# Kernel tuning notes

Measured on AMD Instinct MI355X. Metric: run time of the kernel, lower is better.

Reference implementation:

```python
import jax, jax.numpy as jnp
import numpy as np

N_NODES = 100000
EMBED_DIM = 128
N_EDGES = 3200000
K_HOPS = 2


def setup_inputs() -> dict:
    key = jax.random.key(0)
    k1, k2, k3, k4, k5, k6 = jax.random.split(key, 6)
    stdv = 1.0 / np.sqrt(EMBED_DIM)
    emb = jax.random.uniform(k1, (N_NODES, EMBED_DIM), jnp.float32, -stdv, stdv)
    emb = emb.at[0].set(0.0)  # padding_idx=0
    W = jax.random.uniform(k2, (EMBED_DIM, EMBED_DIM), jnp.float32, -stdv, stdv)
    b = jnp.zeros((EMBED_DIM,), jnp.float32)
    src = jax.random.randint(k3, (N_EDGES,), 0, N_NODES, jnp.int32)
    dst = jax.random.randint(k4, (N_EDGES,), 0, N_NODES, jnp.int32)
    neg_src = jax.random.randint(k5, (N_EDGES,), 0, N_NODES, jnp.int32)
    neg_dst = jax.random.randint(k6, (N_EDGES,), 0, N_NODES, jnp.int32)
    return {"emb": emb, "W": W, "b": b, "src": src, "dst": dst,
            "neg_src": neg_src, "neg_dst": neg_dst}


def _sgconv(x, src, dst, W, b):
    # DGL SGConv, norm='both': symmetric D^{-1/2} A D^{-1/2}, K hops, then Linear.
    deg = jax.ops.segment_sum(jnp.ones_like(dst, jnp.float32), dst,
                              num_segments=N_NODES)
    norm = jax.lax.rsqrt(jnp.maximum(deg, 1.0))[:, None]  # [N,1]
    h = x
    for _ in range(K_HOPS):
        h = h * norm
        h = jax.ops.segment_sum(h[src], dst, num_segments=N_NODES)
        h = h * norm
    return h @ W.T + b


def _edge_dot(h, s, d):
    # fn.u_dot_v: per-edge dot product -> [E,1]
    return jnp.sum(h[s] * h[d], axis=-1, keepdims=True)


def reference(emb, W, b, src, dst, neg_src, neg_dst):
    h = _sgconv(emb, src, dst, W, b)
    return _edge_dot(h, src, dst), _edge_dot(h, neg_src, neg_dst)
```

## Files before the change

kernel.cpp:

```cpp
#include <hip/hip_runtime.h>

#define EMB 128
#define CAP 128

typedef _Float16 half2_t __attribute__((ext_vector_type(2)));

__device__ inline unsigned short f2bf(float f) {
    union { float f; unsigned u; } v; v.f = f;
    unsigned r = v.u + 0x7FFF + ((v.u >> 16) & 1);
    return (unsigned short)(r >> 16);
}
__device__ inline float bf2f(unsigned short b) {
    union { unsigned u; float f; } v; v.u = ((unsigned)b) << 16;
    return v.f;
}
__device__ inline unsigned short f2h(float f) {
    _Float16 h = (_Float16)f;
    return __builtin_bit_cast(unsigned short, h);
}
__device__ inline float fdot2u(unsigned a, unsigned b, float c) {
#if __has_builtin(__builtin_amdgcn_fdot2)
    return __builtin_amdgcn_fdot2(__builtin_bit_cast(half2_t, a),
                                  __builtin_bit_cast(half2_t, b), c, false);
#else
    half2_t ha = __builtin_bit_cast(half2_t, a);
    half2_t hb = __builtin_bit_cast(half2_t, b);
    return c + (float)ha.x * (float)hb.x + (float)ha.y * (float)hb.y;
#endif
}

__global__ void k_fillb(const int* __restrict__ src, const int* __restrict__ dst,
                        int* __restrict__ cnt, int* __restrict__ cs, int E) {
    int i = blockIdx.x * blockDim.x + threadIdx.x;
    int stride = gridDim.x * blockDim.x;
    for (; i < E; i += stride) {
        const int d = dst[i];
        const int s = src[i];
        int p = atomicAdd(&cnt[d], 1);
        if (p < CAP) cs[((size_t)d << 7) + p] = s;
    }
}

__global__ void k_norm(const int* __restrict__ deg, float* __restrict__ nrm,
                       float* __restrict__ nrm2, int N) {
    int i = blockIdx.x * blockDim.x + threadIdx.x;
    if (i < N) {
        float d = fmaxf((float)deg[i], 1.0f);
        float r = 1.0f / sqrtf(d);
        nrm[i] = r;
        nrm2[i] = r * r;
    }
}

__global__ void k_scale_bf(const float* __restrict__ x, const float* __restrict__ s,
                           unsigned short* __restrict__ o, int total4) {
    int idx = blockIdx.x * blockDim.x + threadIdx.x;
    if (idx < total4) {
        const int node = idx >> 5;
        const float4 v = ((const float4*)x)[idx];
        const float f = s[node];
        ushort4 r;
        r.x = f2bf(v.x * f); r.y = f2bf(v.y * f);
        r.z = f2bf(v.z * f); r.w = f2bf(v.w * f);
        ((ushort4*)o)[idx] = r;
    }
}

__global__ __launch_bounds__(256) void k_hop_bb(const unsigned short* __restrict__ in,
                                                const float* __restrict__ oscale,
                                                const int* __restrict__ deg,
                                                const int* __restrict__ csr,
                                                unsigned short* __restrict__ out, int N) {
    const int l = threadIdx.x & 31;
    int hw = (blockIdx.x * blockDim.x + threadIdx.x) >> 5;
    const int nhw = (gridDim.x * blockDim.x) >> 5;
    for (int i = hw; i < N; i += nhw) {
        const int jb = i << 7;
        const int je = jb + min(deg[i], CAP);
        float ax = 0.f, ay = 0.f, az = 0.f, aw = 0.f;
        int j = jb;
        for (; j + 4 <= je; j += 4) {
            const int c0 = csr[j], c1 = csr[j + 1], c2 = csr[j + 2], c3 = csr[j + 3];
            const ushort4 v0 = *(const ushort4*)&in[(size_t)c0 * EMB + 4 * l];
            const ushort4 v1 = *(const ushort4*)&in[(size_t)c1 * EMB + 4 * l];
            const ushort4 v2 = *(const ushort4*)&in[(size_t)c2 * EMB + 4 * l];
            const ushort4 v3 = *(const ushort4*)&in[(size_t)c3 * EMB + 4 * l];
            ax += bf2f(v0.x) + bf2f(v1.x) + bf2f(v2.x) + bf2f(v3.x);
            ay += bf2f(v0.y) + bf2f(v1.y) + bf2f(v2.y) + bf2f(v3.y);
            az += bf2f(v0.z) + bf2f(v1.z) + bf2f(v2.z) + bf2f(v3.z);
            aw += bf2f(v0.w) + bf2f(v1.w) + bf2f(v2.w) + bf2f(v3.w);
        }
        for (; j < je; ++j) {
            const int c = csr[j];
            const ushort4 v = *(const ushort4*)&in[(size_t)c * EMB + 4 * l];
            ax += bf2f(v.x); ay += bf2f(v.y); az += bf2f(v.z); aw += bf2f(v.w);
        }
        const float s = oscale[i];
        ushort4 o;
        o.x = f2bf(ax * s); o.y = f2bf(ay * s);
        o.z = f2bf(az * s); o.w = f2bf(aw * s);
        *(ushort4*)&out[(size_t)i * EMB + 4 * l] = o;
    }
}

__global__ __launch_bounds__(256) void k_hop_bf(const unsigned short* __restrict__ in,
                                                const float* __restrict__ oscale,
                                                const int* __restrict__ deg,
                                                const int* __restrict__ csr,
                                                float* __restrict__ out, int N) {
    const int l = threadIdx.x & 31;
    int hw = (blockIdx.x * blockDim.x + threadIdx.x) >> 5;
    const int nhw = (gridDim.x * blockDim.x) >> 5;
    for (int i = hw; i < N; i += nhw) {
        const int jb = i << 7;
        const int je = jb + min(deg[i], CAP);
        float ax = 0.f, ay = 0.f, az = 0.f, aw = 0.f;
        int j = jb;
        for (; j + 4 <= je; j += 4) {
            const int c0 = csr[j], c1 = csr[j + 1], c2 = csr[j + 2], c3 = csr[j + 3];
            const ushort4 v0 = *(const ushort4*)&in[(size_t)c0 * EMB + 4 * l];
            const ushort4 v1 = *(const ushort4*)&in[(size_t)c1 * EMB + 4 * l];
            const ushort4 v2 = *(const ushort4*)&in[(size_t)c2 * EMB + 4 * l];
            const ushort4 v3 = *(const ushort4*)&in[(size_t)c3 * EMB + 4 * l];
            ax += bf2f(v0.x) + bf2f(v1.x) + bf2f(v2.x) + bf2f(v3.x);
            ay += bf2f(v0.y) + bf2f(v1.y) + bf2f(v2.y) + bf2f(v3.y);
            az += bf2f(v0.z) + bf2f(v1.z) + bf2f(v2.z) + bf2f(v3.z);
            aw += bf2f(v0.w) + bf2f(v1.w) + bf2f(v2.w) + bf2f(v3.w);
        }
        for (; j < je; ++j) {
            const int c = csr[j];
            const ushort4 v = *(const ushort4*)&in[(size_t)c * EMB + 4 * l];
            ax += bf2f(v.x); ay += bf2f(v.y); az += bf2f(v.z); aw += bf2f(v.w);
        }
        const float s = oscale[i];
        float4 o; o.x = ax * s; o.y = ay * s; o.z = az * s; o.w = aw * s;
        *(float4*)&out[(size_t)i * EMB + 4 * l] = o;
    }
}

#define LIN_RT 128
__global__ __launch_bounds__(256) void k_lin(const float* __restrict__ h,
                                             const float* __restrict__ W,
                                             const float* __restrict__ bias,
                                             unsigned short* __restrict__ y, int N) {
    __shared__ float Wl[128 * 128];
    __shared__ float hl[LIN_RT * 129];
    const int t = threadIdx.x;
    const int r0g = blockIdx.x * LIN_RT;
    const int nv = min(LIN_RT, N - r0g);

    {
        const int j = t & 127, k0 = (t >> 7) * 64;
        #pragma unroll
        for (int c = 0; c < 16; ++c) {
            const float4 v = *(const float4*)&W[j * 128 + k0 + 4 * c];
            Wl[(k0 + 4 * c + 0) * 128 + j] = v.x;
            Wl[(k0 + 4 * c + 1) * 128 + j] = v.y;
            Wl[(k0 + 4 * c + 2) * 128 + j] = v.z;
            Wl[(k0 + 4 * c + 3) * 128 + j] = v.w;
        }
    }
    for (int e = t; e < LIN_RT * 32; e += 256) {
        const int r = e >> 5, q = e & 31;
        float4 v; v.x = 0.f; v.y = 0.f; v.z = 0.f; v.w = 0.f;
        if (r < nv) v = *(const float4*)&h[(size_t)(r0g + r) * EMB + 4 * q];
        hl[r * 129 + 4 * q + 0] = v.x;
        hl[r * 129 + 4 * q + 1] = v.y;
        hl[r * 129 + 4 * q + 2] = v.z;
        hl[r * 129 + 4 * q + 3] = v.w;
    }
    __syncthreads();

    const int tc = t & 15, tr = t >> 4;
    const int rb = tr * 8;
    const int j0 = 4 * tc, j1 = 64 + 4 * tc;
    float acc[8][8];
    #pragma unroll
    for (int a = 0; a < 8; ++a)
        #pragma unroll
        for (int b = 0; b < 8; ++b) acc[a][b] = 0.f;

    #pragma unroll 2
    for (int k = 0; k < 128; ++k) {
        const float4 w0 = *(const float4*)&Wl[k * 128 + j0];
        const float4 w1 = *(const float4*)&Wl[k * 128 + j1];
        float hreg[8];
        #pragma unroll
        for (int a = 0; a < 8; ++a) hreg[a] = hl[(rb + a) * 129 + k];
        #pragma unroll
        for (int a = 0; a < 8; ++a) {
            acc[a][0] += hreg[a] * w0.x; acc[a][1] += hreg[a] * w0.y;
            acc[a][2] += hreg[a] * w0.z; acc[a][3] += hreg[a] * w0.w;
            acc[a][4] += hreg[a] * w1.x; acc[a][5] += hreg[a] * w1.y;
            acc[a][6] += hreg[a] * w1.z; acc[a][7] += hreg[a] * w1.w;
        }
    }

    const float4 b0 = *(const float4*)&bias[j0];
    const float4 b1 = *(const float4*)&bias[j1];
    #pragma unroll
    for (int a = 0; a < 8; ++a) {
        const int r = rb + a;
        if (r < nv) {
            ushort4 p0, p1;
            p0.x = f2h(acc[a][0] + b0.x); p0.y = f2h(acc[a][1] + b0.y);
            p0.z = f2h(acc[a][2] + b0.z); p0.w = f2h(acc[a][3] + b0.w);
            p1.x = f2h(acc[a][4] + b1.x); p1.y = f2h(acc[a][5] + b1.y);
            p1.z = f2h(acc[a][6] + b1.z); p1.w = f2h(acc[a][7] + b1.w);
            *(ushort4*)&y[(size_t)(r0g + r) * EMB + j0] = p0;
            *(ushort4*)&y[(size_t)(r0g + r) * EMB + j1] = p1;
        }
    }
}

__global__ __launch_bounds__(256) void k_dot(const unsigned short* __restrict__ y_,
                                             const int* __restrict__ src,
                                             const int* __restrict__ dst,
                                             const int* __restrict__ nsrc,
                                             const int* __restrict__ ndst,
                                             float* __restrict__ out, int E) {
    const uint4* y = (const uint4*)y_;
    const int lane = threadIdx.x & 63;
    const int grp = lane >> 4;
    const int l = lane & 15;
    int w = (blockIdx.x * blockDim.x + threadIdx.x) >> 6;
    const int nw = (gridDim.x * blockDim.x) >> 6;
    const int total = 2 * E;
    const int Q = (total + 3) >> 2;
    for (int q = w; q < Q; q += nw) {
        const int e = 4 * q + grp;
        if (e < total) {
            int s, d;
            if (e < E) { s = src[e]; d = dst[e]; }
            else       { s = nsrc[e - E]; d = ndst[e - E]; }
            const uint4 a = y[(size_t)s * 16 + l];
            const uint4 c = y[(size_t)d * 16 + l];
            float v0 = fdot2u(a.x, c.x, 0.f);
            float v1 = fdot2u(a.y, c.y, 0.f);
            v0 = fdot2u(a.z, c.z, v0);
            v1 = fdot2u(a.w, c.w, v1);
            float v = v0 + v1;
            v += __shfl_xor(v, 8);
            v += __shfl_xor(v, 4);
            v += __shfl_xor(v, 2);
            v += __shfl_xor(v, 1);
            if (l == 0) out[e] = v;
        }
    }
}

extern "C" void kernel_launch(void* const* d_in, const int* in_sizes, int n_in,
                              void* d_out, int out_size, void* d_ws, size_t ws_size,
                              hipStream_t stream) {
    const float* emb = (const float*)d_in[0];
    const float* W   = (const float*)d_in[1];
    const float* bia = (const float*)d_in[2];
    const int* src   = (const int*)d_in[3];
    const int* dst   = (const int*)d_in[4];
    const int* nsrc  = (const int*)d_in[5];
    const int* ndst  = (const int*)d_in[6];
    const int N = in_sizes[0] / EMB;
    const int E = in_sizes[3];
    float* out = (float*)d_out;

    const size_t szBF = (size_t)N * EMB * sizeof(unsigned short);
    const size_t szF  = (size_t)N * EMB * sizeof(float);
    const size_t szN  = (size_t)N * sizeof(int);
    const size_t szCS = (size_t)N * CAP * sizeof(int);

    char* p = (char*)d_ws;
    auto alloc = [&](size_t bytes) { char* r = p; p += (bytes + 255) & ~(size_t)255; return r; };
    unsigned short* X0  = (unsigned short*)alloc(szBF);
    unsigned short* H1  = (unsigned short*)alloc(szBF);
    float*          H2  = (float*)alloc(szF);
    int*   csr  = (int*)alloc(szCS);
    float* nrm  = (float*)alloc(szN);
    float* nrm2 = (float*)alloc(szN);
    int*   cnt  = (int*)alloc(szN);
    unsigned short* ybf = X0;

    hipMemsetAsync(cnt, 0, szN, stream);
    k_fillb<<<2048, 256, 0, stream>>>(src, dst, cnt, csr, E);
    k_norm<<<(N + 255) / 256, 256, 0, stream>>>(cnt, nrm, nrm2, N);

    const int HW_BLOCKS = (N * 32 + 255) / 256;
    k_scale_bf<<<(N * 32 + 255) / 256, 256, 0, stream>>>(emb, nrm, X0, N * 32);
    k_hop_bb<<<HW_BLOCKS, 256, 0, stream>>>(X0, nrm2, cnt, csr, H1, N);
    k_hop_bf<<<HW_BLOCKS, 256, 0, stream>>>(H1, nrm, cnt, csr, H2, N);
    k_lin<<<(N + LIN_RT - 1) / LIN_RT, 256, 0, stream>>>(H2, W, bia, ybf, N);

    k_dot<<<8192, 256, 0, stream>>>(ybf, src, dst, nsrc, ndst, out, E);
}
```

Measured before the change: 997.7 us.

## Split feature dimension into two halves to shrink gather working sets

Stores node features as two separate 64-column halves and runs each propagation hop and edge-dot pass once per half. Each gather pass then touches a table half the size, which is meant to raise L2/MALL hit rates for the random neighbor gathers. It also pads the degree counters to a stride of four ints, presumably to cut atomic contention on shared cache lines. In exchange the CSR indices and edge lists are read twice and there are more kernel launches.

```diff
diff --git a/kernel.cpp b/kernel.cpp
--- a/kernel.cpp
+++ b/kernel.cpp
@@ -2,6 +2,7 @@
 
 #define EMB 128
 #define CAP 128
+#define CSTRIDE 4
 
 typedef _Float16 half2_t __attribute__((ext_vector_type(2)));
 
@@ -36,16 +37,16 @@
     for (; i < E; i += stride) {
         const int d = dst[i];
         const int s = src[i];
-        int p = atomicAdd(&cnt[d], 1);
+        int p = atomicAdd(&cnt[(size_t)d * CSTRIDE], 1);
         if (p < CAP) cs[((size_t)d << 7) + p] = s;
     }
 }
 
-__global__ void k_norm(const int* __restrict__ deg, float* __restrict__ nrm,
+__global__ void k_norm(const int* __restrict__ cnt, float* __restrict__ nrm,
                        float* __restrict__ nrm2, int N) {
     int i = blockIdx.x * blockDim.x + threadIdx.x;
     if (i < N) {
-        float d = fmaxf((float)deg[i], 1.0f);
+        float d = fmaxf((float)cnt[(size_t)i * CSTRIDE], 1.0f);
         float r = 1.0f / sqrtf(d);
         nrm[i] = r;
         nrm2[i] = r * r;
@@ -53,93 +54,94 @@
 }
 
 __global__ void k_scale_bf(const float* __restrict__ x, const float* __restrict__ s,
-                           unsigned short* __restrict__ o, int total4) {
+                           ushort4* __restrict__ o, int N, int total4) {
     int idx = blockIdx.x * blockDim.x + threadIdx.x;
     if (idx < total4) {
         const int node = idx >> 5;
+        const int q = idx & 31;
+        const int h = q >> 4;
+        const int qh = q & 15;
         const float4 v = ((const float4*)x)[idx];
         const float f = s[node];
         ushort4 r;
         r.x = f2bf(v.x * f); r.y = f2bf(v.y * f);
         r.z = f2bf(v.z * f); r.w = f2bf(v.w * f);
-        ((ushort4*)o)[idx] = r;
-    }
-}
-
-__global__ __launch_bounds__(256) void k_hop_bb(const unsigned short* __restrict__ in,
+        o[((size_t)h * N + node) * 16 + qh] = r;
+    }
+}
+
+__global__ __launch_bounds__(256) void k_hop_bb(const ushort4* __restrict__ in_h,
                                                 const float* __restrict__ oscale,
-                                                const int* __restrict__ deg,
+                                                const int* __restrict__ cnt,
                                                 const int* __restrict__ csr,
-                                                unsigned short* __restrict__ out, int N) {
-    const int l = threadIdx.x & 31;
-    int hw = (blockIdx.x * blockDim.x + threadIdx.x) >> 5;
-    const int nhw = (gridDim.x * blockDim.x) >> 5;
-    for (int i = hw; i < N; i += nhw) {
+                                                ushort4* __restrict__ out_h, int N) {
+    const int l = threadIdx.x & 15;
+    int nd = (blockIdx.x * blockDim.x + threadIdx.x) >> 4;
+    const int nnd = (gridDim.x * blockDim.x) >> 4;
+    for (int i = nd; i < N; i += nnd) {
         const int jb = i << 7;
-        const int je = jb + min(deg[i], CAP);
+        const int je = jb + min(cnt[(size_t)i * CSTRIDE], CAP);
         float ax = 0.f, ay = 0.f, az = 0.f, aw = 0.f;
         int j = jb;
         for (; j + 4 <= je; j += 4) {
             const int c0 = csr[j], c1 = csr[j + 1], c2 = csr[j + 2], c3 = csr[j + 3];
-            const ushort4 v0 = *(const ushort4*)&in[(size_t)c0 * EMB + 4 * l];
-            const ushort4 v1 = *(const ushort4*)&in[(size_t)c1 * EMB + 4 * l];
-            const ushort4 v2 = *(const ushort4*)&in[(size_t)c2 * EMB + 4 * l];
-            const ushort4 v3 = *(const ushort4*)&in[(size_t)c3 * EMB + 4 * l];
+            const ushort4 v0 = in_h[(size_t)c0 * 16 + l];
+            const ushort4 v1 = in_h[(size_t)c1 * 16 + l];
+            const ushort4 v2 = in_h[(size_t)c2 * 16 + l];
+            const ushort4 v3 = in_h[(size_t)c3 * 16 + l];
             ax += bf2f(v0.x) + bf2f(v1.x) + bf2f(v2.x) + bf2f(v3.x);
             ay += bf2f(v0.y) + bf2f(v1.y) + bf2f(v2.y) + bf2f(v3.y);
             az += bf2f(v0.z) + bf2f(v1.z) + bf2f(v2.z) + bf2f(v3.z);
             aw += bf2f(v0.w) + bf2f(v1.w) + bf2f(v2.w) + bf2f(v3.w);
         }
         for (; j < je; ++j) {
-            const int c = csr[j];
-            const ushort4 v = *(const ushort4*)&in[(size_t)c * EMB + 4 * l];
+            const ushort4 v = in_h[(size_t)csr[j] * 16 + l];
             ax += bf2f(v.x); ay += bf2f(v.y); az += bf2f(v.z); aw += bf2f(v.w);
         }
         const float s = oscale[i];
         ushort4 o;
         o.x = f2bf(ax * s); o.y = f2bf(ay * s);
         o.z = f2bf(az * s); o.w = f2bf(aw * s);
-        *(ushort4*)&out[(size_t)i * EMB + 4 * l] = o;
-    }
-}
-
-__global__ __launch_bounds__(256) void k_hop_bf(const unsigned short* __restrict__ in,
+        out_h[(size_t)i * 16 + l] = o;
+    }
+}
+
+__global__ __launch_bounds__(256) void k_hop_bf(const ushort4* __restrict__ in_h,
                                                 const float* __restrict__ oscale,
-                                                const int* __restrict__ deg,
+                                                const int* __restrict__ cnt,
                                                 const int* __restrict__ csr,
-                                                float* __restrict__ out, int N) {
-    const int l = threadIdx.x & 31;
-    int hw = (blockIdx.x * blockDim.x + threadIdx.x) >> 5;
-    const int nhw = (gridDim.x * blockDim.x) >> 5;
-    for (int i = hw; i < N; i += nhw) {
+                                                float4* __restrict__ out_h, int N) {
+    const int l = threadIdx.x & 15;
+    int nd = (blockIdx.x * blockDim.x + threadIdx.x) >> 4;
+    const int nnd = (gridDim.x * blockDim.x) >> 4;
+    for (int i = nd; i < N; i += nnd) {
         const int jb = i << 7;
-        const int je = jb + min(deg[i], CAP);
+        const int je = jb + min(cnt[(size_t)i * CSTRIDE], CAP);
         float ax = 0.f, ay = 0.f, az = 0.f, aw = 0.f;
         int j = jb;
         for (; j + 4 <= je; j += 4) {
             const int c0 = csr[j], c1 = csr[j + 1], c2 = csr[j + 2], c3 = csr[j + 3];
-            const ushort4 v0 = *(const ushort4*)&in[(size_t)c0 * EMB + 4 * l];
-            const ushort4 v1 = *(const ushort4*)&in[(size_t)c1 * EMB + 4 * l];
-            const ushort4 v2 = *(const ushort4*)&in[(size_t)c2 * EMB + 4 * l];
-            const ushort4 v3 = *(const ushort4*)&in[(size_t)c3 * EMB + 4 * l];
+            const ushort4 v0 = in_h[(size_t)c0 * 16 + l];
+            const ushort4 v1 = in_h[(size_t)c1 * 16 + l];
+            const ushort4 v2 = in_h[(size_t)c2 * 16 + l];
+            const ushort4 v3 = in_h[(size_t)c3 * 16 + l];
             ax += bf2f(v0.x) + bf2f(v1.x) + bf2f(v2.x) + bf2f(v3.x);
             ay += bf2f(v0.y) + bf2f(v1.y) + bf2f(v2.y) + bf2f(v3.y);
             az += bf2f(v0.z) + bf2f(v1.z) + bf2f(v2.z) + bf2f(v3.z);
             aw += bf2f(v0.w) + bf2f(v1.w) + bf2f(v2.w) + bf2f(v3.w);
         }
         for (; j < je; ++j) {
-            const int c = csr[j];
-            const ushort4 v = *(const ushort4*)&in[(size_t)c * EMB + 4 * l];
+            const ushort4 v = in_h[(size_t)csr[j] * 16 + l];
             ax += bf2f(v.x); ay += bf2f(v.y); az += bf2f(v.z); aw += bf2f(v.w);
         }
         const float s = oscale[i];
         float4 o; o.x = ax * s; o.y = ay * s; o.z = az * s; o.w = aw * s;
-        *(float4*)&out[(size_t)i * EMB + 4 * l] = o;
+        out_h[(size_t)i * 16 + l] = o;
     }
 }
 
 #define LIN_RT 128
-__global__ __launch_bounds__(256) void k_lin(const float* __restrict__ h,
+__global__ __launch_bounds__(256) void k_lin(const float* __restrict__ H2,
                                              const float* __restrict__ W,
                                              const float* __restrict__ bias,
                                              unsigned short* __restrict__ y, int N) {
@@ -148,6 +150,8 @@
     const int t = threadIdx.x;
     const int r0g = blockIdx.x * LIN_RT;
     const int nv = min(LIN_RT, N - r0g);
+    const float* H2_0 = H2;
+    const float* H2_1 = H2 + (size_t)N * 64;
 
     {
         const int j = t & 127, k0 = (t >> 7) * 64;
@@ -163,7 +167,10 @@
     for (int e = t; e < LIN_RT * 32; e += 256) {
         const int r = e >> 5, q = e & 31;
         float4 v; v.x = 0.f; v.y = 0.f; v.z = 0.f; v.w = 0.f;
-        if (r < nv) v = *(const float4*)&h[(size_t)(r0g + r) * EMB + 4 * q];
+        if (r < nv) {
+            if (q < 16) v = *(const float4*)&H2_0[(size_t)(r0g + r) * 64 + 4 * q];
+            else        v = *(const float4*)&H2_1[(size_t)(r0g + r) * 64 + 4 * (q - 16)];
+        }
         hl[r * 129 + 4 * q + 0] = v.x;
         hl[r * 129 + 4 * q + 1] = v.y;
         hl[r * 129 + 4 * q + 2] = v.z;
@@ -196,6 +203,8 @@
         }
     }
 
+    ushort4* y0 = (ushort4*)y;
+    ushort4* y1 = (ushort4*)(y + (size_t)N * 64);
     const float4 b0 = *(const float4*)&bias[j0];
     const float4 b1 = *(const float4*)&bias[j1];
     #pragma unroll
@@ -207,44 +216,43 @@
             p0.z = f2h(acc[a][2] + b0.z); p0.w = f2h(acc[a][3] + b0.w);
             p1.x = f2h(acc[a][4] + b1.x); p1.y = f2h(acc[a][5] + b1.y);
             p1.z = f2h(acc[a][6] + b1.z); p1.w = f2h(acc[a][7] + b1.w);
-            *(ushort4*)&y[(size_t)(r0g + r) * EMB + j0] = p0;
-            *(ushort4*)&y[(size_t)(r0g + r) * EMB + j1] = p1;
-        }
-    }
-}
-
-__global__ __launch_bounds__(256) void k_dot(const unsigned short* __restrict__ y_,
-                                             const int* __restrict__ src,
-                                             const int* __restrict__ dst,
-                                             const int* __restrict__ nsrc,
-                                             const int* __restrict__ ndst,
-                                             float* __restrict__ out, int E) {
-    const uint4* y = (const uint4*)y_;
+            y0[(size_t)(r0g + r) * 16 + tc] = p0;
+            y1[(size_t)(r0g + r) * 16 + tc] = p1;
+        }
+    }
+}
+
+__global__ __launch_bounds__(256) void k_dot_h(const uint4* __restrict__ yh,
+                                               const int* __restrict__ src,
+                                               const int* __restrict__ dst,
+                                               const int* __restrict__ nsrc,
+                                               const int* __restrict__ ndst,
+                                               float* __restrict__ out, int E,
+                                               int accum) {
     const int lane = threadIdx.x & 63;
-    const int grp = lane >> 4;
-    const int l = lane & 15;
+    const int grp = lane >> 3;
+    const int l = lane & 7;
     int w = (blockIdx.x * blockDim.x + threadIdx.x) >> 6;
     const int nw = (gridDim.x * blockDim.x) >> 6;
     const int total = 2 * E;
-    const int Q = (total + 3) >> 2;
+    const int Q = (total + 7) >> 3;
     for (int q = w; q < Q; q += nw) {
-        const int e = 4 * q + grp;
+        const int e = 8 * q + grp;
         if (e < total) {
             int s, d;
             if (e < E) { s = src[e]; d = dst[e]; }
             else       { s = nsrc[e - E]; d = ndst[e - E]; }
-            const uint4 a = y[(size_t)s * 16 + l];
-            const uint4 c = y[(size_t)d * 16 + l];
+            const uint4 a = yh[(size_t)s * 8 + l];
+            const uint4 c = yh[(size_t)d * 8 + l];
             float v0 = fdot2u(a.x, c.x, 0.f);
             float v1 = fdot2u(a.y, c.y, 0.f);
             v0 = fdot2u(a.z, c.z, v0);
             v1 = fdot2u(a.w, c.w, v1);
             float v = v0 + v1;
-            v += __shfl_xor(v, 8);
             v += __shfl_xor(v, 4);
             v += __shfl_xor(v, 2);
             v += __shfl_xor(v, 1);
-            if (l == 0) out[e] = v;
+            if (l == 0) out[e] = accum ? (out[e] + v) : v;
         }
     }
 }
@@ -265,8 +273,8 @@
 
     const size_t szBF = (size_t)N * EMB * sizeof(unsigned short);
     const size_t szF  = (size_t)N * EMB * sizeof(float);
+    const size_t szCS = (size_t)N * CAP * sizeof(int);
     const size_t szN  = (size_t)N * sizeof(int);
-    const size_t szCS = (size_t)N * CAP * sizeof(int);
 
     char* p = (char*)d_ws;
     auto alloc = [&](size_t bytes) { char* r = p; p += (bytes + 255) & ~(size_t)255; return r; };
@@ -276,18 +284,32 @@
     int*   csr  = (int*)alloc(szCS);
     float* nrm  = (float*)alloc(szN);
     float* nrm2 = (float*)alloc(szN);
-    int*   cnt  = (int*)alloc(szN);
+    int*   cnt  = (int*)alloc(szN * CSTRIDE);
     unsigned short* ybf = X0;
 
-    hipMemsetAsync(cnt, 0, szN, stream);
+    hipMemsetAsync(cnt, 0, szN * CSTRIDE, stream);
     k_fillb<<<2048, 256, 0, stream>>>(src, dst, cnt, csr, E);
     k_norm<<<(N + 255) / 256, 256, 0, stream>>>(cnt, nrm, nrm2, N);
 
-    const int HW_BLOCKS = (N * 32 + 255) / 256;
-    k_scale_bf<<<(N * 32 + 255) / 256, 256, 0, stream>>>(emb, nrm, X0, N * 32);
-    k_hop_bb<<<HW_BLOCKS, 256, 0, stream>>>(X0, nrm2, cnt, csr, H1, N);
-    k_hop_bf<<<HW_BLOCKS, 256, 0, stream>>>(H1, nrm, cnt, csr, H2, N);
+    const int total4 = N * 32;
+    k_scale_bf<<<(total4 + 255) / 256, 256, 0, stream>>>(emb, nrm, (ushort4*)X0, N, total4);
+
+    const int ND_BLOCKS = (N * 16 + 255) / 256;
+    const ushort4* X0u = (const ushort4*)X0;
+    ushort4* H1u = (ushort4*)H1;
+    float4* H2u = (float4*)H2;
+    for (int h = 0; h < 2; ++h)
+        k_hop_bb<<<ND_BLOCKS, 256, 0, stream>>>(X0u + (size_t)h * N * 16, nrm2, cnt, csr,
+                                                H1u + (size_t)h * N * 16, N);
+    for (int h = 0; h < 2; ++h)
+        k_hop_bf<<<ND_BLOCKS, 256, 0, stream>>>((const ushort4*)H1 + (size_t)h * N * 16,
+                                                nrm, cnt, csr,
+                                                H2u + (size_t)h * N * 16, N);
+
     k_lin<<<(N + LIN_RT - 1) / LIN_RT, 256, 0, stream>>>(H2, W, bia, ybf, N);
 
-    k_dot<<<8192, 256, 0, stream>>>(ybf, src, dst, nsrc, ndst, out, E);
-}
+    const uint4* y0 = (const uint4*)ybf;
+    const uint4* y1 = (const uint4*)(ybf + (size_t)N * 64);
+    k_dot_h<<<8192, 256, 0, stream>>>(y0, src, dst, nsrc, ndst, out, E, 0);
+    k_dot_h<<<8192, 256, 0, stream>>>(y1, src, dst, nsrc, ndst, out, E, 1);
+}
```

Result: faster. 962.0 us (-3.6%).
